# Kernel tuning notes

Measured on AMD Instinct MI355X. Metric: run time of the kernel, lower is better.

The kernel has to match this reference:

```python
import jax, jax.numpy as jnp
import numpy as np

N_NODES = 100000
N_EDGES = 1600000
N_HIDDEN = 128
EPS = 1e-12  # F.normalize default eps


def setup_inputs() -> dict:
    key = jax.random.key(0)
    k1, k2, k3, k4 = jax.random.split(key, 4)
    emb = jax.random.normal(k1, (N_NODES, N_HIDDEN), dtype=jnp.float32)
    d = jnp.ones((N_HIDDEN,), dtype=jnp.float32)          # nn.Parameter ones
    scale = jnp.full((1,), 0.5, dtype=jnp.float32)        # nn.Parameter 0.5
    src = jax.random.randint(k2, (N_EDGES,), 0, N_NODES)
    dst = jax.random.randint(k3, (N_EDGES,), 0, N_NODES)
    return {"emb": emb, "d": d, "scale": scale, "src": src, "dst": dst}


def reference(emb, d, scale, src, dst):
    # L2 normalize rows (torch F.normalize: x / max(||x||, eps))
    norm = jnp.sqrt(jnp.sum(emb * emb, axis=1, keepdims=True))
    e = emb / jnp.maximum(norm, EPS)            # [N, H]
    ew = e * d                                   # emb @ diag(d), as elementwise scale
    # u_dot_v: per-edge dot product of src 'ew' and dst 'e' -> [E, 1]
    z = jnp.sum(ew[src] * e[dst], axis=-1, keepdims=True)
    return z * scale
```

## Files before the change

### kernel.cpp

```cpp
#include <hip/hip_runtime.h>

#define HIDDEN 128
#define EPS 1e-12f

__device__ __forceinline__ int pack4(float x, float y, float z, float w, float s) {
    int q0 = (int)rintf(x * s);
    int q1 = (int)rintf(y * s);
    int q2 = (int)rintf(z * s);
    int q3 = (int)rintf(w * s);
    return (q0 & 255) | ((q1 & 255) << 8) | ((q2 & 255) << 16) | (q3 << 24);
}

__device__ __forceinline__ int dot4i8(int a, int b, int c) {
#if __has_builtin(__builtin_amdgcn_sdot4)
    return __builtin_amdgcn_sdot4(a, b, c, false);
#else
    int r = c;
    r += ((a << 24) >> 24) * ((b << 24) >> 24);
    r += ((a << 16) >> 24) * ((b << 16) >> 24);
    r += ((a <<  8) >> 24) * ((b <<  8) >> 24);
    r += (a >> 24) * (b >> 24);
    return r;
#endif
}

__global__ __launch_bounds__(256) void normalize_quant_kernel(
    const float* __restrict__ emb, const float* __restrict__ d,
    int* __restrict__ q, float* __restrict__ sf, int* __restrict__ mp,
    int n_nodes) {
    if (blockIdx.x == 0 && threadIdx.x < 32) {
        const float* dd = d + threadIdx.x * 4;
        int m = 0;
        if (dd[0] >= 0.0f) m |= 0x000000FF;
        if (dd[1] >= 0.0f) m |= 0x0000FF00;
        if (dd[2] >= 0.0f) m |= 0x00FF0000;
        if (dd[3] >= 0.0f) m |= 0xFF000000;
        mp[threadIdx.x] = m;
    }

    int row  = blockIdx.x * 8 + (threadIdx.x >> 5);
    if (row >= n_nodes) return;
    int lane = threadIdx.x & 31;

    float4 v = ((const float4*)emb)[(size_t)row * 32 + lane];
    float ss = v.x * v.x + v.y * v.y + v.z * v.z + v.w * v.w;
    #pragma unroll
    for (int m = 16; m >= 1; m >>= 1) ss += __shfl_xor(ss, m);
    float inv = 1.0f / fmaxf(sqrtf(ss), EPS);

    float4 d4 = ((const float4*)d)[lane];
    float4 f4;
    f4.x = sqrtf(fabsf(d4.x)); f4.y = sqrtf(fabsf(d4.y));
    f4.z = sqrtf(fabsf(d4.z)); f4.w = sqrtf(fabsf(d4.w));

    float4 w4;
    w4.x = v.x * inv * f4.x; w4.y = v.y * inv * f4.y;
    w4.z = v.z * inv * f4.z; w4.w = v.w * inv * f4.w;

    float mw = fmaxf(fmaxf(fabsf(w4.x), fabsf(w4.y)), fmaxf(fabsf(w4.z), fabsf(w4.w)));
    #pragma unroll
    for (int m = 16; m >= 1; m >>= 1) mw = fmaxf(mw, __shfl_xor(mw, m));

    float inv_w = mw > 0.0f ? 127.0f / mw : 0.0f;
    q[(size_t)row * 32 + lane] = pack4(w4.x, w4.y, w4.z, w4.w, inv_w);
    if (lane == 0) sf[row] = mw * (1.0f / 127.0f);
}

__global__ __launch_bounds__(256) void edge_dot_kernel(
    const int* __restrict__ q, const float* __restrict__ sf,
    const float* __restrict__ scale, const int* __restrict__ src,
    const int* __restrict__ dst, const int* __restrict__ mp,
    float* __restrict__ out, int n_edges) {
    int group = blockIdx.x * 32 + (threadIdx.x >> 3);
    int lane  = threadIdx.x & 7;
    int base  = group * 4;
    if (base >= n_edges) return;

    int4 maskp = ((const int4*)mp)[lane];
    int4 maskn;
    maskn.x = ~maskp.x; maskn.y = ~maskp.y; maskn.z = ~maskp.z; maskn.w = ~maskp.w;

    int s[4], t[4];
    if (base + 3 < n_edges) {
        int4 s4 = ((const int4*)src)[group];
        int4 t4 = ((const int4*)dst)[group];
        s[0] = s4.x; s[1] = s4.y; s[2] = s4.z; s[3] = s4.w;
        t[0] = t4.x; t[1] = t4.y; t[2] = t4.z; t[3] = t4.w;
    } else {
        #pragma unroll
        for (int j = 0; j < 4; ++j) {
            int e = min(base + j, n_edges - 1);
            s[j] = src[e]; t[j] = dst[e];
        }
    }

    int4 a[4], b[4];
    #pragma unroll
    for (int j = 0; j < 4; ++j) {
        a[j] = ((const int4*)q)[(size_t)s[j] * 8 + lane];
        b[j] = ((const int4*)q)[(size_t)t[j] * 8 + lane];
    }

    float r0 = 0.0f; int ss = 0, tt = 0;
    #pragma unroll
    for (int j = 0; j < 4; ++j) {
        int p = 0, n = 0;
        p = dot4i8(a[j].x & maskp.x, b[j].x, p);
        n = dot4i8(a[j].x & maskn.x, b[j].x, n);
        p = dot4i8(a[j].y & maskp.y, b[j].y, p);
        n = dot4i8(a[j].y & maskn.y, b[j].y, n);
        p = dot4i8(a[j].z & maskp.z, b[j].z, p);
        n = dot4i8(a[j].z & maskn.z, b[j].z, n);
        p = dot4i8(a[j].w & maskp.w, b[j].w, p);
        n = dot4i8(a[j].w & maskn.w, b[j].w, n);
        int acc = p - n;
        #pragma unroll
        for (int m = 4; m >= 1; m >>= 1) acc += __shfl_xor(acc, m);
        if (lane == j) { r0 = (float)acc; ss = s[j]; tt = t[j]; }
    }

    int e = base + lane;
    if (lane < 4 && e < n_edges)
        out[e] = r0 * sf[ss] * sf[tt] * scale[0];
}

extern "C" void kernel_launch(void* const* d_in, const int* in_sizes, int n_in,
                              void* d_out, int out_size, void* d_ws, size_t ws_size,
                              hipStream_t stream) {
    const float* emb   = (const float*)d_in[0];
    const float* d     = (const float*)d_in[1];
    const float* scale = (const float*)d_in[2];
    const int*   src   = (const int*)d_in[3];
    const int*   dst   = (const int*)d_in[4];
    float*       out   = (float*)d_out;

    int n_nodes = in_sizes[0] / HIDDEN;
    int n_edges = in_sizes[3];

    int*   q  = (int*)d_ws;
    float* sf = (float*)(q + (size_t)n_nodes * 32);
    int*   mp = (int*)(sf + n_nodes);

    int blocks1 = (n_nodes + 7) / 8;
    normalize_quant_kernel<<<blocks1, 256, 0, stream>>>(emb, d, q, sf, mp, n_nodes);

    int blocks2 = (n_edges + 127) / 128;
    edge_dot_kernel<<<blocks2, 256, 0, stream>>>(q, sf, scale, src, dst, mp, out, n_edges);
}
```

Before: 146.8 us.

## Software-pipeline edge gathers in persistent grid-stride edge-dot kernel

```diff
diff --git a/kernel.cpp b/kernel.cpp
--- a/kernel.cpp
+++ b/kernel.cpp
@@ -66,62 +66,99 @@
     if (lane == 0) sf[row] = mw * (1.0f / 127.0f);
 }
 
-__global__ __launch_bounds__(256) void edge_dot_kernel(
+
+#define LOAD_IDX(gq, sv, tv) do {                                             \
+    int base_ = (gq) << 2;                                                    \
+    if (base_ + 3 < n_edges) {                                                \
+        int4 s4_ = ((const int4*)src)[gq];                                    \
+        int4 t4_ = ((const int4*)dst)[gq];                                    \
+        sv[0] = s4_.x; sv[1] = s4_.y; sv[2] = s4_.z; sv[3] = s4_.w;           \
+        tv[0] = t4_.x; tv[1] = t4_.y; tv[2] = t4_.z; tv[3] = t4_.w;           \
+    } else {                                                                  \
+        _Pragma("unroll")                                                     \
+        for (int j_ = 0; j_ < 4; ++j_) {                                      \
+            int e_ = min(base_ + j_, n_edges - 1);                            \
+            sv[j_] = src[e_]; tv[j_] = dst[e_];                               \
+        }                                                                     \
+    }                                                                         \
+} while (0)
+
+#define GATHER(sv, tv, aa, bb, fs, ft) do {                                   \
+    _Pragma("unroll")                                                         \
+    for (int j_ = 0; j_ < 4; ++j_) {                                          \
+        aa[j_] = q4[(size_t)sv[j_] * 8 + lane];                               \
+        bb[j_] = q4[(size_t)tv[j_] * 8 + lane];                               \
+    }                                                                         \
+    fs = sf[sv[lane & 3]];                                                    \
+    ft = sf[tv[lane & 3]];                                                    \
+} while (0)
+
+#define COMPUTE_STORE(gq, aa, bb, fs, ft) do {                                \
+    float r0_ = 0.0f;                                                         \
+    _Pragma("unroll")                                                         \
+    for (int j_ = 0; j_ < 4; ++j_) {                                          \
+        int p_ = 0, n_ = 0;                                                   \
+        p_ = dot4i8(aa[j_].x & maskp.x, bb[j_].x, p_);                        \
+        n_ = dot4i8(aa[j_].x & maskn.x, bb[j_].x, n_);                        \
+        p_ = dot4i8(aa[j_].y & maskp.y, bb[j_].y, p_);                        \
+        n_ = dot4i8(aa[j_].y & maskn.y, bb[j_].y, n_);                        \
+        p_ = dot4i8(aa[j_].z & maskp.z, bb[j_].z, p_);                        \
+        n_ = dot4i8(aa[j_].z & maskn.z, bb[j_].z, n_);                        \
+        p_ = dot4i8(aa[j_].w & maskp.w, bb[j_].w, p_);                        \
+        n_ = dot4i8(aa[j_].w & maskn.w, bb[j_].w, n_);                        \
+        int acc_ = p_ - n_;                                                   \
+        _Pragma("unroll")                                                     \
+        for (int m_ = 4; m_ >= 1; m_ >>= 1) acc_ += __shfl_xor(acc_, m_);     \
+        if (lane == j_) r0_ = (float)acc_;                                    \
+    }                                                                         \
+    int e_ = ((gq) << 2) + lane;                                              \
+    if (lane < 4 && e_ < n_edges) out[e_] = r0_ * (fs) * (ft) * sc;           \
+} while (0)
+
+__global__ __launch_bounds__(256, 4) void edge_dot_kernel(
     const int* __restrict__ q, const float* __restrict__ sf,
     const float* __restrict__ scale, const int* __restrict__ src,
     const int* __restrict__ dst, const int* __restrict__ mp,
-    float* __restrict__ out, int n_edges) {
-    int group = blockIdx.x * 32 + (threadIdx.x >> 3);
-    int lane  = threadIdx.x & 7;
-    int base  = group * 4;
-    if (base >= n_edges) return;
+    float* __restrict__ out, int n_edges, int n_tiles) {
+    const int lane = threadIdx.x & 7;
+    const int grp  = threadIdx.x >> 3;
+    const int gstride = gridDim.x * 32;
+    const int4* q4 = (const int4*)q;
 
     int4 maskp = ((const int4*)mp)[lane];
     int4 maskn;
     maskn.x = ~maskp.x; maskn.y = ~maskp.y; maskn.z = ~maskp.z; maskn.w = ~maskp.w;
+    const float sc = scale[0];
 
-    int s[4], t[4];
-    if (base + 3 < n_edges) {
-        int4 s4 = ((const int4*)src)[group];
-        int4 t4 = ((const int4*)dst)[group];
-        s[0] = s4.x; s[1] = s4.y; s[2] = s4.z; s[3] = s4.w;
-        t[0] = t4.x; t[1] = t4.y; t[2] = t4.z; t[3] = t4.w;
-    } else {
-        #pragma unroll
-        for (int j = 0; j < 4; ++j) {
-            int e = min(base + j, n_edges - 1);
-            s[j] = src[e]; t[j] = dst[e];
-        }
+    int g = blockIdx.x * 32 + grp;
+    if (g >= n_tiles) return;
+
+    int sA[4], tA[4], sB[4], tB[4];
+    int4 aA[4], bA[4], aB[4], bB[4];
+    float fsA, ftA, fsB, ftB;
+
+    LOAD_IDX(g, sA, tA);
+    GATHER(sA, tA, aA, bA, fsA, ftA);
+    {
+        int g1 = g + gstride;
+        if (g1 < n_tiles) LOAD_IDX(g1, sB, tB);
     }
 
-    int4 a[4], b[4];
-    #pragma unroll
-    for (int j = 0; j < 4; ++j) {
-        a[j] = ((const int4*)q)[(size_t)s[j] * 8 + lane];
-        b[j] = ((const int4*)q)[(size_t)t[j] * 8 + lane];
+    for (;;) {
+        int gB = g + gstride;
+        if (gB >= n_tiles) { COMPUTE_STORE(g, aA, bA, fsA, ftA); break; }
+        GATHER(sB, tB, aB, bB, fsB, ftB);
+        { int g2 = gB + gstride; if (g2 < n_tiles) LOAD_IDX(g2, sA, tA); }
+        COMPUTE_STORE(g, aA, bA, fsA, ftA);
+        g = gB;
+
+        gB = g + gstride;
+        if (gB >= n_tiles) { COMPUTE_STORE(g, aB, bB, fsB, ftB); break; }
+        GATHER(sA, tA, aA, bA, fsA, ftA);
+        { int g2 = gB + gstride; if (g2 < n_tiles) LOAD_IDX(g2, sB, tB); }
+        COMPUTE_STORE(g, aB, bB, fsB, ftB);
+        g = gB;
     }
-
-    float r0 = 0.0f; int ss = 0, tt = 0;
-    #pragma unroll
-    for (int j = 0; j < 4; ++j) {
-        int p = 0, n = 0;
-        p = dot4i8(a[j].x & maskp.x, b[j].x, p);
-        n = dot4i8(a[j].x & maskn.x, b[j].x, n);
-        p = dot4i8(a[j].y & maskp.y, b[j].y, p);
-        n = dot4i8(a[j].y & maskn.y, b[j].y, n);
-        p = dot4i8(a[j].z & maskp.z, b[j].z, p);
-        n = dot4i8(a[j].z & maskn.z, b[j].z, n);
-        p = dot4i8(a[j].w & maskp.w, b[j].w, p);
-        n = dot4i8(a[j].w & maskn.w, b[j].w, n);
-        int acc = p - n;
-        #pragma unroll
-        for (int m = 4; m >= 1; m >>= 1) acc += __shfl_xor(acc, m);
-        if (lane == j) { r0 = (float)acc; ss = s[j]; tt = t[j]; }
-    }
-
-    int e = base + lane;
-    if (lane < 4 && e < n_edges)
-        out[e] = r0 * sf[ss] * sf[tt] * scale[0];
 }
 
 extern "C" void kernel_launch(void* const* d_in, const int* in_sizes, int n_in,
@@ -144,6 +181,9 @@
     int blocks1 = (n_nodes + 7) / 8;
     normalize_quant_kernel<<<blocks1, 256, 0, stream>>>(emb, d, q, sf, mp, n_nodes);
 
-    int blocks2 = (n_edges + 127) / 128;
-    edge_dot_kernel<<<blocks2, 256, 0, stream>>>(q, sf, scale, src, dst, mp, out, n_edges);
+    int n_tiles = (n_edges + 3) >> 2;
+    int blocks2 = (n_tiles + 31) / 32;
+    if (blocks2 > 1024) blocks2 = 1024;
+    edge_dot_kernel<<<blocks2, 256, 0, stream>>>(q, sf, scale, src, dst, mp,
+                                                 out, n_edges, n_tiles);
 }
```

After: 149.0 us. Within noise of the previous version (+1.5%).
